# Performance work log

Hardware: AMD Instinct MI355X
Metric: run time of the kernel (lower is better)

Reference implementation:

```python
import jax, jax.numpy as jnp
from jax import lax
import numpy as np


def _conv(x, w, b, stride=1, pad=0):
    # x: NCHW, w: OIHW
    o = lax.conv_general_dilated(x, w, (stride, stride), [(pad, pad), (pad, pad)],
                                 dimension_numbers=('NCHW', 'OIHW', 'NCHW'))
    return o + b[None, :, None, None]


def _up2(x):
    return jnp.repeat(jnp.repeat(x, 2, axis=2), 2, axis=3)


def _boundary_agg(x, w, b):
    # up_to_bottom = prefix-max along H; bottom_to_up = suffix-max along H;
    # left_to_right / right_to_left (via rot90) = prefix/suffix max along W (square spatial).
    x1 = lax.cummax(x, axis=2)
    x2 = lax.cummax(x, axis=2, reverse=True)
    x3 = lax.cummax(x, axis=3)
    x4 = lax.cummax(x, axis=3, reverse=True)
    return _conv(jnp.concatenate([x, x1, x2, x3, x4], axis=1), w, b)


def _forward(C3, C4, C5,
             ba3_w, ba3_b, ba4_w, ba4_b, ba5_w, ba5_b,
             p5_1_w, p5_1_b, p5_1d_w, p5_1d_b, p5_2_w, p5_2_b,
             p4_1_w, p4_1_b, p4_1d_w, p4_1d_b, p4_2_w, p4_2_b,
             p3_1_w, p3_1_b, p3_1d_w, p3_1d_b, p3_2_w, p3_2_b,
             p6_w, p6_b, p7_w, p7_b,
             c34_w, c34_b, c45_w, c45_b, c35_w, c35_b,
             gamma3, gamma4, gamma5):
    C3_BA = _boundary_agg(C3, ba3_w, ba3_b)
    C4_BA = _boundary_agg(C4, ba4_w, ba4_b)
    C5_BA = _boundary_agg(C5, ba5_w, ba5_b)
    # top-down path
    P5 = _conv(C5, p5_1_w, p5_1_b)
    P5u1 = _up2(P5)
    P5u2 = _up2(P5u1)
    P5 = _conv(P5, p5_2_w, p5_2_b, 1, 1)
    P4 = _conv(C4, p4_1_w, p4_1_b) + P5u1
    P4u1 = _up2(P4)
    P4 = _conv(P4, p4_2_w, p4_2_b, 1, 1)
    P3 = _conv(C3, p3_1_w, p3_1_b) + P4u1 + P5u2
    P3 = _conv(P3, p3_2_w, p3_2_b, 1, 1)
    # bottom-up (dual) path on boundary-aggregated features
    P3d = _conv(C3_BA, p3_1d_w, p3_1d_b)
    P3d1 = _conv(P3d, c34_w, c34_b, 2, 1)   # 3x3 s2 p1
    P3d2 = _conv(P3d1, c35_w, c35_b, 2, 0)  # 2x2 s2 p0
    P4d = _conv(C4_BA, p4_1d_w, p4_1d_b) + P3d1
    P4d1 = _conv(P4d, c45_w, c45_b, 2, 0)   # 2x2 s2 p0
    P5d = _conv(C5_BA, p5_1d_w, p5_1d_b) + P4d1 + P3d2
    # extra levels
    P6 = _conv(C5, p6_w, p6_b, 2, 1)
    P7 = _conv(jax.nn.relu(P6), p7_w, p7_b, 2, 1)
    # gated merge
    O3 = gamma3 * P3d + (1.0 - gamma3) * P3
    O4 = gamma4 * P4d + (1.0 - gamma4) * P4
    O5 = gamma5 * P5d + (1.0 - gamma5) * P5
    return (O3, O4, O5, P6, P7)


def setup_inputs() -> dict:
    key = jax.random.key(0)
    ks = iter(jax.random.split(key, 48))
    def rnd(shape, scale):
        return jax.random.normal(next(ks), shape, dtype=jnp.float32) * scale
    B, F = 8, 256
    d = {
        'C3': rnd((B, 256, 64, 64), 1.0),
        'C4': rnd((B, 512, 32, 32), 1.0),
        'C5': rnd((B, 1024, 16, 16), 1.0),
        # Boundary_Aggregation 1x1 convs: in_channels*5 -> in_channels
        'ba3_w': rnd((256, 1280, 1, 1), 0.02), 'ba3_b': rnd((256,), 0.02),
        'ba4_w': rnd((512, 2560, 1, 1), 0.02), 'ba4_b': rnd((512,), 0.02),
        'ba5_w': rnd((1024, 5120, 1, 1), 0.01), 'ba5_b': rnd((1024,), 0.02),
        # FPN lateral / smoothing convs
        'p5_1_w': rnd((F, 1024, 1, 1), 0.02), 'p5_1_b': rnd((F,), 0.02),
        'p5_1d_w': rnd((F, 1024, 1, 1), 0.02), 'p5_1d_b': rnd((F,), 0.02),
        'p5_2_w': rnd((F, F, 3, 3), 0.02), 'p5_2_b': rnd((F,), 0.02),
        'p4_1_w': rnd((F, 512, 1, 1), 0.02), 'p4_1_b': rnd((F,), 0.02),
        'p4_1d_w': rnd((F, 512, 1, 1), 0.02), 'p4_1d_b': rnd((F,), 0.02),
        'p4_2_w': rnd((F, F, 3, 3), 0.02), 'p4_2_b': rnd((F,), 0.02),
        'p3_1_w': rnd((F, 256, 1, 1), 0.02), 'p3_1_b': rnd((F,), 0.02),
        'p3_1d_w': rnd((F, 256, 1, 1), 0.02), 'p3_1d_b': rnd((F,), 0.02),
        'p3_2_w': rnd((F, F, 3, 3), 0.02), 'p3_2_b': rnd((F,), 0.02),
        'p6_w': rnd((F, 1024, 3, 3), 0.02), 'p6_b': rnd((F,), 0.02),
        'p7_w': rnd((F, F, 3, 3), 0.02), 'p7_b': rnd((F,), 0.02),
        # downsample convs in dual path
        'c34_w': rnd((F, F, 3, 3), 0.02), 'c34_b': rnd((F,), 0.02),
        'c45_w': rnd((F, F, 2, 2), 0.02), 'c45_b': rnd((F,), 0.02),
        'c35_w': rnd((F, F, 2, 2), 0.02), 'c35_b': rnd((F,), 0.02),
        'gamma3': rnd((1,), 0.3), 'gamma4': rnd((1,), 0.3), 'gamma5': rnd((1,), 0.3),
    }
    return d


def reference(C3, C4, C5,
              ba3_w, ba3_b, ba4_w, ba4_b, ba5_w, ba5_b,
              p5_1_w, p5_1_b, p5_1d_w, p5_1d_b, p5_2_w, p5_2_b,
              p4_1_w, p4_1_b, p4_1d_w, p4_1d_b, p4_2_w, p4_2_b,
              p3_1_w, p3_1_b, p3_1d_w, p3_1d_b, p3_2_w, p3_2_b,
              p6_w, p6_b, p7_w, p7_b,
              c34_w, c34_b, c45_w, c45_b, c35_w, c35_b,
              gamma3, gamma4, gamma5):
    return _forward(C3, C4, C5,
                    ba3_w, ba3_b, ba4_w, ba4_b, ba5_w, ba5_b,
                    p5_1_w, p5_1_b, p5_1d_w, p5_1d_b, p5_2_w, p5_2_b,
                    p4_1_w, p4_1_b, p4_1d_w, p4_1d_b, p4_2_w, p4_2_b,
                    p3_1_w, p3_1_b, p3_1d_w, p3_1d_b, p3_2_w, p3_2_b,
                    p6_w, p6_b, p7_w, p7_b,
                    c34_w, c34_b, c45_w, c45_b, c35_w, c35_b,
                    gamma3, gamma4, gamma5)
```

## Files before the change

kernel.cpp:

```cpp
#include <hip/hip_runtime.h>

typedef unsigned short u16;
typedef __attribute__((ext_vector_type(8))) short s8v;
typedef __attribute__((ext_vector_type(4))) float f4v;

__device__ __forceinline__ u16 f2bf(float f) {
  unsigned int x = __float_as_uint(f);
  return (u16)((x + 0x7fffu + ((x >> 16) & 1u)) >> 16);
}
__device__ __forceinline__ float bf2f(u16 u) {
  return __uint_as_float(((unsigned int)u) << 16);
}
__device__ __forceinline__ void gload16(const void* g, void* l) {
  __builtin_amdgcn_global_load_lds(
      (const __attribute__((address_space(1))) void*)g,
      (__attribute__((address_space(3))) void*)l, 16, 0, 0);
}

struct Epi {
  const float* bias;
  const u16* r1; int r1Hp, r1pad, r1sh;
  const u16* r2; int r2Hp, r2pad, r2sh;
  const float* gamma; const u16* other; int oHp, opad, gmode;
  u16* outB; int oBHp, oBpad, oBrelu;
  float* outF;
};

__device__ __forceinline__ size_t nhwc_idx(int b, int h, int w, int Hp, int pad, int Cc, int m) {
  return (((size_t)(b * Hp + h + pad)) * Hp + (w + pad)) * Cc + m;
}

__device__ __forceinline__ void epi_apply_store(float v, int m, int b, int oh, int ow,
                                                int p, int M, int l2ohow, float g, const Epi& ep) {
  if (ep.bias) v += ep.bias[m];
  if (ep.r1) v += bf2f(ep.r1[nhwc_idx(b, oh >> ep.r1sh, ow >> ep.r1sh, ep.r1Hp, ep.r1pad, 256, m)]);
  if (ep.r2) v += bf2f(ep.r2[nhwc_idx(b, oh >> ep.r2sh, ow >> ep.r2sh, ep.r2Hp, ep.r2pad, 256, m)]);
  if (ep.gmode) {
    float o = bf2f(ep.other[nhwc_idx(b, oh, ow, ep.oHp, ep.opad, 256, m)]);
    v = (ep.gmode == 1) ? (g * o + (1.f - g) * v) : (g * v + (1.f - g) * o);
  }
  if (ep.outF) ep.outF[(((size_t)(b * M + m)) << l2ohow) + p] = v;
  if (ep.outB) {
    float w = ep.oBrelu ? fmaxf(v, 0.f) : v;
    ep.outB[nhwc_idx(b, oh, ow, ep.oBHp, ep.oBpad, M, m)] = f2bf(w);
  }
}

__device__ __forceinline__ void epi4(f4v a, int mbase, int b, int oh, int ow,
                                     int p, int M, int l2ohow, float g, const Epi& ep) {
  float v[4];
#pragma unroll
  for (int r = 0; r < 4; ++r) v[r] = a[r];
  if (ep.bias) {
    const float* bp = &ep.bias[mbase];
#pragma unroll
    for (int r = 0; r < 4; ++r) v[r] += bp[r];
  }
  if (ep.r1) {
    const u16* rp = &ep.r1[nhwc_idx(b, oh >> ep.r1sh, ow >> ep.r1sh, ep.r1Hp, ep.r1pad, 256, mbase)];
#pragma unroll
    for (int r = 0; r < 4; ++r) v[r] += bf2f(rp[r]);
  }
  if (ep.r2) {
    const u16* rp = &ep.r2[nhwc_idx(b, oh >> ep.r2sh, ow >> ep.r2sh, ep.r2Hp, ep.r2pad, 256, mbase)];
#pragma unroll
    for (int r = 0; r < 4; ++r) v[r] += bf2f(rp[r]);
  }
  if (ep.gmode) {
    const u16* op = &ep.other[nhwc_idx(b, oh, ow, ep.oHp, ep.opad, 256, mbase)];
#pragma unroll
    for (int r = 0; r < 4; ++r) {
      float o = bf2f(op[r]);
      v[r] = (ep.gmode == 1) ? (g * o + (1.f - g) * v[r]) : (g * v[r] + (1.f - g) * o);
    }
  }
  if (ep.outF) {
    float* fp = &ep.outF[(((size_t)(b * M + mbase)) << l2ohow) + p];
#pragma unroll
    for (int r = 0; r < 4; ++r) fp[(size_t)r << l2ohow] = v[r];
  }
  if (ep.outB) {
    u16* obp = &ep.outB[nhwc_idx(b, oh, ow, ep.oBHp, ep.oBpad, M, mbase)];
    ushort4 pk;
    if (ep.oBrelu) { pk.x = f2bf(fmaxf(v[0], 0.f)); pk.y = f2bf(fmaxf(v[1], 0.f));
                     pk.z = f2bf(fmaxf(v[2], 0.f)); pk.w = f2bf(fmaxf(v[3], 0.f)); }
    else { pk.x = f2bf(v[0]); pk.y = f2bf(v[1]); pk.z = f2bf(v[2]); pk.w = f2bf(v[3]); }
    *(ushort4*)obp = pk;
  }
}

struct WSeg { const float* src; u16* dst; int K, l2Cin, mode, ktiles, blk0; };
struct WTab { WSeg s[17]; };

__global__ __launch_bounds__(256) void k_cvt_w(WTab tab) {
  int bid = blockIdx.x;
  int si = 0;
#pragma unroll
  for (int i = 1; i < 17; ++i) si += (bid >= tab.s[i].blk0) ? 1 : 0;
  WSeg sg = tab.s[si];
  int rel = bid - sg.blk0;
  int m = rel / sg.ktiles;
  int kt = rel - m * sg.ktiles;
  int r = kt * 256 + threadIdx.x;
  if (r >= sg.K) return;
  int Cin = 1 << sg.l2Cin;
  int q = r >> sg.l2Cin, c = r & (Cin - 1);
  int sidx;
  if (sg.mode == 1) {
    int og = (q < 4) ? (q + 1) : 0;
    sidx = m * sg.K + og * Cin + c;
  } else {
    int KHW = sg.K >> sg.l2Cin;
    sidx = (m * Cin + c) * KHW + q;
  }
  sg.dst[(size_t)m * sg.K + r] = f2bf(sg.src[sidx]);
}

__global__ __launch_bounds__(256) void k_cvt_x(const float* __restrict__ in, u16* __restrict__ out,
                                               int C, int H, int W, int Hp, int P, int tw) {
  __shared__ u16 tile[32][33];
  const int t = threadIdx.x;
  const int b = blockIdx.z, h = blockIdx.y;
  const int tc = blockIdx.x / tw, twi = blockIdx.x - tc * tw;
  const int c0 = tc * 32, w0 = twi * 32;
#pragma unroll
  for (int r = 0; r < 4; ++r) {
    int cl = (t >> 5) * 4 + r, wl = t & 31;
    if (w0 + wl < W) tile[cl][wl] = f2bf(in[(((size_t)b * C + c0 + cl) * H + h) * W + w0 + wl]);
  }
  __syncthreads();
#pragma unroll
  for (int r = 0; r < 4; ++r) {
    int wl = (t >> 5) * 4 + r, cl = t & 31;
    if (w0 + wl < W) out[(((size_t)(b * Hp + h + P)) * Hp + (w0 + wl + P)) * C + c0 + cl] = tile[cl][wl];
  }
}

template<int S, int L2S>
__global__ __launch_bounds__(256) void k_scan2(const float* __restrict__ x,
                                               u16* __restrict__ out, int l2C) {
  __shared__ u16 pl[S][S + 1], rp[S][S + 1], rs[S][S + 1];
  const int pid = blockIdx.x;
  const size_t SS = (size_t)S * S;
  const size_t GS = ((size_t)8 << l2C) * SS;
  const float* xp = x + (size_t)pid * SS;
  u16* g0 = out + (size_t)pid * SS;
  u16* g1 = g0 + GS;
  u16* g2 = g1 + GS;
  u16* g3 = g2 + GS;
  const int t = threadIdx.x;
  for (int idx = t; idx < S * S; idx += 256)
    pl[idx >> L2S][idx & (S - 1)] = f2bf(xp[idx]);
  __syncthreads();
  if (t < S) {
    float m = -INFINITY;
    for (int h = 0; h < S; ++h) { m = fmaxf(m, bf2f(pl[h][t])); g0[h * S + t] = f2bf(m); }
  } else if (t < 2 * S) {
    int c = t - S;
    float m = -INFINITY;
    for (int h = S - 1; h >= 0; --h) { m = fmaxf(m, bf2f(pl[h][c])); g1[h * S + c] = f2bf(m); }
  } else if (t < 3 * S) {
    int h = t - 2 * S;
    float m = -INFINITY;
    for (int w = 0; w < S; ++w) { m = fmaxf(m, bf2f(pl[h][w])); rp[h][w] = f2bf(m); }
  } else if (t < 4 * S) {
    int h = t - 3 * S;
    float m = -INFINITY;
    for (int w = S - 1; w >= 0; --w) { m = fmaxf(m, bf2f(pl[h][w])); rs[h][w] = f2bf(m); }
  }
  __syncthreads();
  for (int idx = t; idx < S * S; idx += 256) {
    g2[idx] = rp[idx >> L2S][idx & (S - 1)];
    g3[idx] = rs[idx >> L2S][idx & (S - 1)];
  }
}

__global__ __launch_bounds__(256) void k_tr(const u16* __restrict__ src, u16* __restrict__ dst,
                                            int C, int S, int tw) {
  __shared__ u16 tile[32][33];
  const int t = threadIdx.x;
  const int z = blockIdx.z, h = blockIdx.y;
  const int tc = blockIdx.x / tw, twi = blockIdx.x - tc * tw;
  const int c0 = tc * 32, w0 = twi * 32;
  const size_t SS = (size_t)S * S;
  const u16* sp = src + (size_t)z * C * SS;
  u16* dp = dst + (size_t)z * SS * C;
#pragma unroll
  for (int r = 0; r < 4; ++r) {
    int cl = (t >> 5) * 4 + r, wl = t & 31;
    if (w0 + wl < S) tile[cl][wl] = sp[(size_t)(c0 + cl) * SS + h * S + w0 + wl];
  }
  __syncthreads();
#pragma unroll
  for (int r = 0; r < 4; ++r) {
    int wl = (t >> 5) * 4 + r, cl = t & 31;
    if (w0 + wl < S) dp[((size_t)(h * S + w0 + wl)) * C + c0 + cl] = tile[cl][wl];
  }
}

template<int QDIV, int KW, int STR, bool FUSE>
__global__ __launch_bounds__(256)
void k_gemm(const u16* __restrict__ X, const u16* __restrict__ X2,
            const u16* __restrict__ Wt,
            float* __restrict__ part, int C, int l2C, int Hp, int ipad,
            int l2ohow, int l2ow, int K, int Ksp, int M, int N, Epi ep) {
  __shared__ u16 Al[4096];
  __shared__ u16 Bl[8192];
  const int tid = threadIdx.x, lane = tid & 63, wid = tid >> 6;

  int ntile, mtile;
  {
    const int NT = gridDim.x, MT = gridDim.y;
    int nm = blockIdx.x + NT * blockIdx.y;
    if ((NT & 7) == 0) {
      int low = nm & 7, r = nm >> 3;
      mtile = r % MT;
      ntile = ((r / MT) << 3) + low;
    } else { ntile = blockIdx.x; mtile = blockIdx.y; }
  }
  const int n0 = ntile * 128, m0 = mtile * 64;
  const int kb = blockIdx.z * Ksp;
  const int mw = (wid >> 1) * 32, nw = (wid & 1) * 64;

  const int srow = lane >> 2;
  const int schunk = (lane & 3) ^ ((srow >> 1) & 3);

  const u16* pa0 = Wt + (size_t)(m0 + wid * 16 + srow) * K + kb + schunk * 8;

  const u16* pb0 = nullptr; const u16* pb1 = nullptr;
  int rowB[2], ohsB[2], owsB[2];
  int q = 0, cnt = 0, khs = 0, kws = 0;
#pragma unroll
  for (int j = 0; j < 2; ++j) {
    int n = n0 + wid * 32 + j * 16 + srow;
    int b = n >> l2ohow, p = n & ((1 << l2ohow) - 1);
    int oh = p >> l2ow, ow = p & ((1 << l2ow) - 1);
    if (QDIV == 1) {
      const u16* gg = X + ((size_t)(b * Hp + oh + ipad) * Hp + (ow + ipad)) * C + kb + schunk * 8;
      if (j == 0) pb0 = gg; else pb1 = gg;
    } else if (QDIV == 5) {
      rowB[j] = n;
    } else {
      rowB[j] = b * Hp; ohsB[j] = oh * STR + ipad; owsB[j] = ow * STR + ipad;
    }
  }
  if (QDIV == 5) {
    q = kb >> l2C;
    int c0 = kb & (C - 1);
    cnt = (C - c0) >> 5;
    const u16* base = (q < 4) ? (X + (((size_t)q << Hp) << l2C)) : X2;
    pb0 = base + (((size_t)rowB[0]) << l2C) + c0 + schunk * 8;
    pb1 = base + (((size_t)rowB[1]) << l2C) + c0 + schunk * 8;
  } else if (QDIV != 1) {
    q = kb >> l2C;
    int c0 = kb & (C - 1);
    cnt = (C - c0) >> 5;
    if (QDIV == 4) { khs = q >> 1; kws = q & 1; } else { khs = q / 3; kws = q - khs * 3; }
    pb0 = X + ((size_t)(rowB[0] + ohsB[0] + khs) * Hp + (owsB[0] + kws)) * C + c0 + schunk * 8;
    pb1 = X + ((size_t)(rowB[1] + ohsB[1] + khs) * Hp + (owsB[1] + kws)) * C + c0 + schunk * 8;
  }

  f4v acc[2][4];
#pragma unroll
  for (int i = 0; i < 2; ++i)
#pragma unroll
    for (int j = 0; j < 4; ++j) acc[i][j] = (f4v){0.f, 0.f, 0.f, 0.f};

  const int fr = lane & 15, kc = lane >> 4;
  const int fxor = (kc ^ ((fr >> 1) & 3)) * 8;

  auto advB = [&]() {
    if (QDIV == 1) { pb0 += 32; pb1 += 32; }
    else if (--cnt == 0) {
      ++q; cnt = C >> 5;
      if (QDIV == 5) {
        const u16* base = (q < 4) ? (X + (((size_t)q << Hp) << l2C)) : X2;
        pb0 = base + (((size_t)rowB[0]) << l2C) + schunk * 8;
        pb1 = base + (((size_t)rowB[1]) << l2C) + schunk * 8;
      } else {
        if (++kws == KW) { kws = 0; ++khs; }
        pb0 = X + ((size_t)(rowB[0] + ohsB[0] + khs) * Hp + (owsB[0] + kws)) * C + schunk * 8;
        pb1 = X + ((size_t)(rowB[1] + ohsB[1] + khs) * Hp + (owsB[1] + kws)) * C + schunk * 8;
      }
    } else { pb0 += 32; pb1 += 32; }
  };
  auto stage = [&](int buf) {
    u16* la = Al + buf * 2048 + wid * 512;
    u16* lb = Bl + buf * 4096 + wid * 1024;
    gload16(pa0, la);
    gload16(pb0, lb); gload16(pb1, lb + 512);
    pa0 += 32;
    advB();
  };

  const int nt = Ksp >> 5;
  stage(0);
  for (int t = 0; t < nt; ++t) {
    const int cur = t & 1;
    if (t + 1 < nt) {
      stage(cur ^ 1);
      asm volatile("s_waitcnt vmcnt(3)" ::: "memory");
    } else {
      asm volatile("s_waitcnt vmcnt(0)" ::: "memory");
    }
    __builtin_amdgcn_s_barrier();
    asm volatile("" ::: "memory");
    const u16* ca = Al + cur * 2048;
    const u16* cb = Bl + cur * 4096;
    s8v a[2], bv[4];
#pragma unroll
    for (int mf = 0; mf < 2; ++mf) a[mf] = *(const s8v*)&ca[(mw + mf * 16 + fr) * 32 + fxor];
#pragma unroll
    for (int nf = 0; nf < 4; ++nf) bv[nf] = *(const s8v*)&cb[(nw + nf * 16 + fr) * 32 + fxor];
#pragma unroll
    for (int mf = 0; mf < 2; ++mf)
#pragma unroll
      for (int nf = 0; nf < 4; ++nf)
        acc[mf][nf] = __builtin_amdgcn_mfma_f32_16x16x32_bf16(a[mf], bv[nf], acc[mf][nf], 0, 0, 0);
    __builtin_amdgcn_s_barrier();
    asm volatile("" ::: "memory");
  }

  const int r4 = kc * 4;
  if (FUSE) {
    float g = ep.gmode ? *ep.gamma : 0.f;
#pragma unroll
    for (int nf = 0; nf < 4; ++nf) {
      int n = n0 + nw + nf * 16 + fr;
      int b = n >> l2ohow, p = n & ((1 << l2ohow) - 1);
      int oh = p >> l2ow, ow = p & ((1 << l2ow) - 1);
#pragma unroll
      for (int mf = 0; mf < 2; ++mf)
        epi4(acc[mf][nf], m0 + mw + mf * 16 + r4, b, oh, ow, p, M, l2ohow, g, ep);
    }
  } else {
#pragma unroll
    for (int mf = 0; mf < 2; ++mf)
#pragma unroll
      for (int r = 0; r < 4; ++r) {
        int m = m0 + mw + mf * 16 + r4 + r;
        float* pr = part + ((size_t)blockIdx.z * M + m) * N + n0 + nw + fr;
#pragma unroll
        for (int nf = 0; nf < 4; ++nf) pr[nf * 16] = acc[mf][nf][r];
      }
  }
}

__global__ __launch_bounds__(256) void k_red(const float* __restrict__ part, int z, int M,
                                             int l2N, int l2ohow, int l2ow, Epi ep) {
  size_t MN = ((size_t)M) << l2N;
  int N = 1 << l2N;
  float g = ep.gmode ? *ep.gamma : 0.f;
  for (size_t e = (size_t)blockIdx.x * 256 + threadIdx.x; e < MN; e += (size_t)gridDim.x * 256) {
    float v = 0.f;
    for (int s = 0; s < z; ++s) v += part[(size_t)s * MN + e];
    int m = (int)(e >> l2N), n = (int)(e & (N - 1));
    int b = n >> l2ohow, p = n & ((1 << l2ohow) - 1);
    int oh = p >> l2ow, ow = p & ((1 << l2ow) - 1);
    epi_apply_store(v, m, b, oh, ow, p, M, l2ohow, g, ep);
  }
}

static const size_t WR_BA3 = 0, WR_BA4 = 327680, WR_BA5 = 1638400,
  WR_P51 = 6881280, WR_P51D = 7143424, WR_P52 = 7405568, WR_P41 = 7995392,
  WR_P41D = 8126464, WR_P42 = 8257536, WR_P31 = 8847360, WR_P31D = 8912896,
  WR_P32 = 8978432, WR_P6 = 9568256, WR_P7 = 11927552, WR_C34 = 12517376,
  WR_C45 = 13107200, WR_C35 = 13369344;
static const size_t O_C3N = 13631488, O_C4N = 22020096, O_C5N = 26214400,
  O_C3BA = 28311552, O_C4BA = 36700160, O_C5BA = 40894464,
  O_CAT = 42991616, O_SCR = 76546048;
static const size_t O_P3D = O_CAT, O_P3PRE = O_CAT + 8921088,
  O_P4PRE = O_CAT + 17842176, O_P3D1 = O_CAT + 20209664,
  O_P4D = O_CAT + 22306816, O_P4D1 = O_CAT + 24403968,
  O_P3D2 = O_CAT + 24928256, O_P5PRE = O_CAT + 25452544,
  O_P5S = O_CAT + 26116096, O_P6R = O_CAT + 26640384, O_C5P = O_CAT + 26845184;

extern "C" void kernel_launch(void* const* d_in, const int* in_sizes, int n_in,
                              void* d_out, int out_size, void* d_ws, size_t ws_size,
                              hipStream_t stream) {
  (void)in_sizes; (void)n_in; (void)out_size; (void)ws_size;
  const float* C3 = (const float*)d_in[0];
  const float* C4 = (const float*)d_in[1];
  const float* C5 = (const float*)d_in[2];
  const float* ba3_w = (const float*)d_in[3];  const float* ba3_b = (const float*)d_in[4];
  const float* ba4_w = (const float*)d_in[5];  const float* ba4_b = (const float*)d_in[6];
  const float* ba5_w = (const float*)d_in[7];  const float* ba5_b = (const float*)d_in[8];
  const float* p5_1_w = (const float*)d_in[9];  const float* p5_1_b = (const float*)d_in[10];
  const float* p5_1d_w = (const float*)d_in[11]; const float* p5_1d_b = (const float*)d_in[12];
  const float* p5_2_w = (const float*)d_in[13]; const float* p5_2_b = (const float*)d_in[14];
  const float* p4_1_w = (const float*)d_in[15]; const float* p4_1_b = (const float*)d_in[16];
  const float* p4_1d_w = (const float*)d_in[17]; const float* p4_1d_b = (const float*)d_in[18];
  const float* p4_2_w = (const float*)d_in[19]; const float* p4_2_b = (const float*)d_in[20];
  const float* p3_1_w = (const float*)d_in[21]; const float* p3_1_b = (const float*)d_in[22];
  const float* p3_1d_w = (const float*)d_in[23]; const float* p3_1d_b = (const float*)d_in[24];
  const float* p3_2_w = (const float*)d_in[25]; const float* p3_2_b = (const float*)d_in[26];
  const float* p6_w = (const float*)d_in[27]; const float* p6_b = (const float*)d_in[28];
  const float* p7_w = (const float*)d_in[29]; const float* p7_b = (const float*)d_in[30];
  const float* c34_w = (const float*)d_in[31]; const float* c34_b = (const float*)d_in[32];
  const float* c45_w = (const float*)d_in[33]; const float* c45_b = (const float*)d_in[34];
  const float* c35_w = (const float*)d_in[35]; const float* c35_b = (const float*)d_in[36];
  const float* g3 = (const float*)d_in[37];
  const float* g4 = (const float*)d_in[38];
  const float* g5 = (const float*)d_in[39];

  float* out = (float*)d_out;
  float* O3 = out;
  float* O4 = out + 8388608;
  float* O5 = out + 10485760;
  float* P6o = out + 11010048;
  float* P7o = out + 11141120;

  u16* wsu = (u16*)d_ws;
  u16* c3n = wsu + O_C3N;  u16* c4n = wsu + O_C4N;  u16* c5n = wsu + O_C5N;
  u16* c3ba = wsu + O_C3BA; u16* c4ba = wsu + O_C4BA; u16* c5ba = wsu + O_C5BA;
  u16* catb = wsu + O_CAT;
  u16* scr = wsu + O_SCR;
  u16* p3d = wsu + O_P3D;  u16* p3d1 = wsu + O_P3D1; u16* p3d2 = wsu + O_P3D2;
  u16* p4d = wsu + O_P4D;  u16* p4d1 = wsu + O_P4D1;
  u16* p5pre = wsu + O_P5PRE; u16* p5s = wsu + O_P5S; u16* p4pre = wsu + O_P4PRE;
  u16* p3pre = wsu + O_P3PRE; u16* p6r = wsu + O_P6R; u16* c5p = wsu + O_C5P;
  float* part = (float*)scr;
  float* partba = (float*)scr;

  const Epi enone = {nullptr, nullptr,0,0,0, nullptr,0,0,0, nullptr,nullptr,0,0,0, nullptr,0,0,0, nullptr};

  WTab tab;
  int ti = 0, blk = 0;
  auto add = [&](const float* s, size_t off, int M, int K, int l2Cin, int mode) {
    int kt = (K + 255) / 256;
    tab.s[ti].src = s; tab.s[ti].dst = wsu + off; tab.s[ti].K = K;
    tab.s[ti].l2Cin = l2Cin; tab.s[ti].mode = mode;
    tab.s[ti].ktiles = kt; tab.s[ti].blk0 = blk;
    blk += M * kt; ++ti;
  };
  add(ba3_w, WR_BA3, 256, 1280, 8, 1);
  add(ba4_w, WR_BA4, 512, 2560, 9, 1);
  add(ba5_w, WR_BA5, 1024, 5120, 10, 1);
  add(p5_1_w, WR_P51, 256, 1024, 10, 0);
  add(p5_1d_w, WR_P51D, 256, 1024, 10, 0);
  add(p5_2_w, WR_P52, 256, 2304, 8, 0);
  add(p4_1_w, WR_P41, 256, 512, 9, 0);
  add(p4_1d_w, WR_P41D, 256, 512, 9, 0);
  add(p4_2_w, WR_P42, 256, 2304, 8, 0);
  add(p3_1_w, WR_P31, 256, 256, 8, 0);
  add(p3_1d_w, WR_P31D, 256, 256, 8, 0);
  add(p3_2_w, WR_P32, 256, 2304, 8, 0);
  add(p6_w, WR_P6, 256, 9216, 10, 0);
  add(p7_w, WR_P7, 256, 2304, 8, 0);
  add(c34_w, WR_C34, 256, 2304, 8, 0);
  add(c45_w, WR_C45, 256, 1024, 8, 0);
  add(c35_w, WR_C35, 256, 1024, 8, 0);
  k_cvt_w<<<blk, 256, 0, stream>>>(tab);

  k_cvt_x<<<dim3(16,64,8), 256, 0, stream>>>(C3, c3n, 256, 64, 64, 64, 0, 2);
  k_cvt_x<<<dim3(16,32,8), 256, 0, stream>>>(C4, c4n, 512, 32, 32, 32, 0, 1);
  k_cvt_x<<<dim3(32,16,8), 256, 0, stream>>>(C5, c5n, 1024, 16, 16, 16, 0, 1);

  k_scan2<64, 6><<<2048, 256, 0, stream>>>(C3, scr, 8);
  k_tr<<<dim3(16,64,32), 256, 0, stream>>>(scr, catb, 256, 64, 2);
  {
    Epi ep = {ba3_b, nullptr,0,0,0, nullptr,0,0,0, nullptr,nullptr,0,0,0, c3ba,64,0,0, nullptr};
    k_gemm<5,1,1,true><<<dim3(256,4,1), 256, 0, stream>>>(
        catb, c3n, wsu + WR_BA3, nullptr, 256, 8, 15, 0, 12, 6, 1280, 1280, 256, 32768, ep);
  }
  k_scan2<32, 5><<<4096, 256, 0, stream>>>(C4, scr, 9);
  k_tr<<<dim3(16,32,32), 256, 0, stream>>>(scr, catb, 512, 32, 1);
  k_gemm<5,1,1,false><<<dim3(64,8,2), 256, 0, stream>>>(
      catb, c4n, wsu + WR_BA4, partba, 512, 9, 13, 0, 10, 5, 2560, 1280, 512, 8192, enone);
  {
    Epi ep = {ba4_b, nullptr,0,0,0, nullptr,0,0,0, nullptr,nullptr,0,0,0, c4ba,32,0,0, nullptr};
    k_red<<<2048, 256, 0, stream>>>(partba, 2, 512, 13, 10, 5, ep);
  }
  k_scan2<16, 4><<<8192, 256, 0, stream>>>(C5, scr, 10);
  k_tr<<<dim3(32,16,32), 256, 0, stream>>>(scr, catb, 1024, 16, 1);
  k_gemm<5,1,1,false><<<dim3(16,16,4), 256, 0, stream>>>(
      catb, c5n, wsu + WR_BA5, partba, 1024, 10, 11, 0, 8, 4, 5120, 1280, 1024, 2048, enone);
  {
    Epi ep = {ba5_b, nullptr,0,0,0, nullptr,0,0,0, nullptr,nullptr,0,0,0, c5ba,16,0,0, nullptr};
    k_red<<<2048, 256, 0, stream>>>(partba, 4, 1024, 11, 8, 4, ep);
  }

  hipMemsetAsync(p3d, 0, (size_t)8921088 * 2, stream);
  hipMemsetAsync(p3pre, 0, (size_t)8921088 * 2, stream);
  hipMemsetAsync(p4pre, 0, (size_t)2367488 * 2, stream);
  hipMemsetAsync(p5pre, 0, (size_t)663552 * 2, stream);
  hipMemsetAsync(p6r, 0, (size_t)204800 * 2, stream);
  hipMemsetAsync(c5p, 0, (size_t)2654208 * 2, stream);
  k_cvt_x<<<dim3(32,16,8), 256, 0, stream>>>(C5, c5p, 1024, 16, 16, 18, 1, 1);

  {
    Epi ep = {p3_1d_b, nullptr,0,0,0, nullptr,0,0,0, nullptr,nullptr,0,0,0, p3d,66,1,0, nullptr};
    k_gemm<1,1,1,true><<<dim3(256,4,1), 256, 0, stream>>>(
        c3ba, nullptr, wsu + WR_P31D, nullptr, 256, 0, 64, 0, 12, 6, 256, 256, 256, 32768, ep);
  }
  k_gemm<9,3,2,false><<<dim3(64,4,4), 256, 0, stream>>>(
      p3d, nullptr, wsu + WR_C34, part, 256, 8, 66, 0, 10, 5, 2304, 576, 256, 8192, enone);
  {
    Epi ep = {c34_b, nullptr,0,0,0, nullptr,0,0,0, nullptr,nullptr,0,0,0, p3d1,32,0,0, nullptr};
    k_red<<<2048, 256, 0, stream>>>(part, 4, 256, 13, 10, 5, ep);
  }
  k_gemm<4,2,2,false><<<dim3(16,4,8), 256, 0, stream>>>(
      p3d1, nullptr, wsu + WR_C35, part, 256, 8, 32, 0, 8, 4, 1024, 128, 256, 2048, enone);
  {
    Epi ep = {c35_b, nullptr,0,0,0, nullptr,0,0,0, nullptr,nullptr,0,0,0, p3d2,16,0,0, nullptr};
    k_red<<<2048, 256, 0, stream>>>(part, 8, 256, 11, 8, 4, ep);
  }
  k_gemm<1,1,1,false><<<dim3(64,4,4), 256, 0, stream>>>(
      c4ba, nullptr, wsu + WR_P41D, part, 512, 0, 32, 0, 10, 5, 512, 128, 256, 8192, enone);
  {
    Epi ep = {p4_1d_b, p3d1,32,0,0, nullptr,0,0,0, nullptr,nullptr,0,0,0, p4d,32,0,0, nullptr};
    k_red<<<2048, 256, 0, stream>>>(part, 4, 256, 13, 10, 5, ep);
  }
  k_gemm<4,2,2,false><<<dim3(16,4,8), 256, 0, stream>>>(
      p4d, nullptr, wsu + WR_C45, part, 256, 8, 32, 0, 8, 4, 1024, 128, 256, 2048, enone);
  {
    Epi ep = {c45_b, nullptr,0,0,0, nullptr,0,0,0, nullptr,nullptr,0,0,0, p4d1,16,0,0, nullptr};
    k_red<<<2048, 256, 0, stream>>>(part, 8, 256, 11, 8, 4, ep);
  }

  k_gemm<1,1,1,false><<<dim3(16,4,8), 256, 0, stream>>>(
      c5n, nullptr, wsu + WR_P51, part, 1024, 0, 16, 0, 8, 4, 1024, 128, 256, 2048, enone);
  {
    Epi ep = {p5_1_b, nullptr,0,0,0, nullptr,0,0,0, nullptr,nullptr,0,0,0, p5pre,18,1,0, nullptr};
    k_red<<<2048, 256, 0, stream>>>(part, 8, 256, 11, 8, 4, ep);
  }
  k_gemm<9,3,1,false><<<dim3(16,4,8), 256, 0, stream>>>(
      p5pre, nullptr, wsu + WR_P52, part, 256, 8, 18, 0, 8, 4, 2304, 288, 256, 2048, enone);
  {
    Epi ep = {p5_2_b, nullptr,0,0,0, nullptr,0,0,0, nullptr,nullptr,0,0,0, p5s,16,0,0, nullptr};
    k_red<<<2048, 256, 0, stream>>>(part, 8, 256, 11, 8, 4, ep);
  }
  k_gemm<1,1,1,false><<<dim3(64,4,4), 256, 0, stream>>>(
      c4n, nullptr, wsu + WR_P41, part, 512, 0, 32, 0, 10, 5, 512, 128, 256, 8192, enone);
  {
    Epi ep = {p4_1_b, p5pre,18,1,1, nullptr,0,0,0, nullptr,nullptr,0,0,0, p4pre,34,1,0, nullptr};
    k_red<<<2048, 256, 0, stream>>>(part, 4, 256, 13, 10, 5, ep);
  }
  k_gemm<9,3,1,false><<<dim3(64,4,4), 256, 0, stream>>>(
      p4pre, nullptr, wsu + WR_P42, part, 256, 8, 34, 0, 10, 5, 2304, 576, 256, 8192, enone);
  {
    Epi ep = {p4_2_b, nullptr,0,0,0, nullptr,0,0,0, g4,p4d,32,0,1, nullptr,0,0,0, O4};
    k_red<<<2048, 256, 0, stream>>>(part, 4, 256, 13, 10, 5, ep);
  }
  {
    Epi ep = {p3_1_b, p4pre,34,1,1, p5pre,18,1,2, nullptr,nullptr,0,0,0, p3pre,66,1,0, nullptr};
    k_gemm<1,1,1,true><<<dim3(256,4,1), 256, 0, stream>>>(
        c3n, nullptr, wsu + WR_P31, nullptr, 256, 0, 64, 0, 12, 6, 256, 256, 256, 32768, ep);
  }
  {
    Epi ep = {p3_2_b, nullptr,0,0,0, nullptr,0,0,0, g3,p3d,66,1,1, nullptr,0,0,0, O3};
    k_gemm<9,3,1,true><<<dim3(256,4,1), 256, 0, stream>>>(
        p3pre, nullptr, wsu + WR_P32, nullptr, 256, 8, 66, 0, 12, 6, 2304, 2304, 256, 32768, ep);
  }
  k_gemm<1,1,1,false><<<dim3(16,4,8), 256, 0, stream>>>(
      c5ba, nullptr, wsu + WR_P51D, part, 1024, 0, 16, 0, 8, 4, 1024, 128, 256, 2048, enone);
  {
    Epi ep = {p5_1d_b, p4d1,16,0,0, p3d2,16,0,0, g5,p5s,16,0,2, nullptr,0,0,0, O5};
    k_red<<<2048, 256, 0, stream>>>(part, 8, 256, 11, 8, 4, ep);
  }

  k_gemm<9,3,2,false><<<dim3(4,4,32), 256, 0, stream>>>(
      c5p, nullptr, wsu + WR_P6, part, 1024, 10, 18, 0, 6, 3, 9216, 288, 256, 512, enone);
  {
    Epi ep = {p6_b, nullptr,0,0,0, nullptr,0,0,0, nullptr,nullptr,0,0,0, p6r,10,1,1, P6o};
    k_red<<<512, 256, 0, stream>>>(part, 32, 256, 9, 6, 3, ep);
  }
  k_gemm<9,3,2,false><<<dim3(1,4,8), 256, 0, stream>>>(
      p6r, nullptr, wsu + WR_P7, part, 256, 8, 10, 0, 4, 2, 2304, 288, 256, 128, enone);
  {
    Epi ep = {p7_b, nullptr,0,0,0, nullptr,0,0,0, nullptr,nullptr,0,0,0, nullptr,0,0,0, P7o};
    k_red<<<128, 256, 0, stream>>>(part, 8, 256, 7, 4, 2, ep);
  }
}
```

Measured before the change: 763.4 us.

## Load GEMM operands directly from global into registers, dropping LDS staging

Removes the shared-memory double buffer and global_load_lds staging in the implicit-GEMM conv kernel. Each wave now loads its own A and B MFMA fragments from global memory into registers, with one-step register prefetch, and drops both barriers per K-step. The cost is redundant global/L2 traffic, because waves that share the same A or B tiles each reload them, and the per-lane 16-byte loads are less coalesced.

```diff
diff --git a/kernel.cpp b/kernel.cpp
--- a/kernel.cpp
+++ b/kernel.cpp
@@ -10,11 +10,6 @@
 }
 __device__ __forceinline__ float bf2f(u16 u) {
   return __uint_as_float(((unsigned int)u) << 16);
-}
-__device__ __forceinline__ void gload16(const void* g, void* l) {
-  __builtin_amdgcn_global_load_lds(
-      (const __attribute__((address_space(1))) void*)g,
-      (__attribute__((address_space(3))) void*)l, 16, 0, 0);
 }
 
 struct Epi {
@@ -204,8 +199,6 @@
             const u16* __restrict__ Wt,
             float* __restrict__ part, int C, int l2C, int Hp, int ipad,
             int l2ohow, int l2ow, int K, int Ksp, int M, int N, Epi ep) {
-  __shared__ u16 Al[4096];
-  __shared__ u16 Bl[8192];
   const int tid = threadIdx.x, lane = tid & 63, wid = tid >> 6;
 
   int ntile, mtile;
@@ -221,27 +214,25 @@
   const int n0 = ntile * 128, m0 = mtile * 64;
   const int kb = blockIdx.z * Ksp;
   const int mw = (wid >> 1) * 32, nw = (wid & 1) * 64;
-
-  const int srow = lane >> 2;
-  const int schunk = (lane & 3) ^ ((srow >> 1) & 3);
-
-  const u16* pa0 = Wt + (size_t)(m0 + wid * 16 + srow) * K + kb + schunk * 8;
-
-  const u16* pb0 = nullptr; const u16* pb1 = nullptr;
-  int rowB[2], ohsB[2], owsB[2];
+  const int fr = lane & 15, kc = lane >> 4;
+
+  const u16* pa0 = Wt + (size_t)(m0 + mw + fr) * K + kb + kc * 8;
+  const u16* pa1 = pa0 + (size_t)16 * K;
+
+  const u16* pb[4];
+  int rowB[4], ohsB[4], owsB[4];
   int q = 0, cnt = 0, khs = 0, kws = 0;
 #pragma unroll
-  for (int j = 0; j < 2; ++j) {
-    int n = n0 + wid * 32 + j * 16 + srow;
+  for (int nf = 0; nf < 4; ++nf) {
+    int n = n0 + nw + nf * 16 + fr;
     int b = n >> l2ohow, p = n & ((1 << l2ohow) - 1);
     int oh = p >> l2ow, ow = p & ((1 << l2ow) - 1);
     if (QDIV == 1) {
-      const u16* gg = X + ((size_t)(b * Hp + oh + ipad) * Hp + (ow + ipad)) * C + kb + schunk * 8;
-      if (j == 0) pb0 = gg; else pb1 = gg;
+      pb[nf] = X + ((size_t)(b * Hp + oh + ipad) * Hp + (ow + ipad)) * C + kb + kc * 8;
     } else if (QDIV == 5) {
-      rowB[j] = n;
+      rowB[nf] = n;
     } else {
-      rowB[j] = b * Hp; ohsB[j] = oh * STR + ipad; owsB[j] = ow * STR + ipad;
+      rowB[nf] = b * Hp; ohsB[nf] = oh * STR + ipad; owsB[nf] = ow * STR + ipad;
     }
   }
   if (QDIV == 5) {
@@ -249,15 +240,17 @@
     int c0 = kb & (C - 1);
     cnt = (C - c0) >> 5;
     const u16* base = (q < 4) ? (X + (((size_t)q << Hp) << l2C)) : X2;
-    pb0 = base + (((size_t)rowB[0]) << l2C) + c0 + schunk * 8;
-    pb1 = base + (((size_t)rowB[1]) << l2C) + c0 + schunk * 8;
+#pragma unroll
+    for (int nf = 0; nf < 4; ++nf)
+      pb[nf] = base + (((size_t)rowB[nf]) << l2C) + c0 + kc * 8;
   } else if (QDIV != 1) {
     q = kb >> l2C;
     int c0 = kb & (C - 1);
     cnt = (C - c0) >> 5;
     if (QDIV == 4) { khs = q >> 1; kws = q & 1; } else { khs = q / 3; kws = q - khs * 3; }
-    pb0 = X + ((size_t)(rowB[0] + ohsB[0] + khs) * Hp + (owsB[0] + kws)) * C + c0 + schunk * 8;
-    pb1 = X + ((size_t)(rowB[1] + ohsB[1] + khs) * Hp + (owsB[1] + kws)) * C + c0 + schunk * 8;
+#pragma unroll
+    for (int nf = 0; nf < 4; ++nf)
+      pb[nf] = X + ((size_t)(rowB[nf] + ohsB[nf] + khs) * Hp + (owsB[nf] + kws)) * C + c0 + kc * 8;
   }
 
   f4v acc[2][4];
@@ -266,60 +259,59 @@
 #pragma unroll
     for (int j = 0; j < 4; ++j) acc[i][j] = (f4v){0.f, 0.f, 0.f, 0.f};
 
-  const int fr = lane & 15, kc = lane >> 4;
-  const int fxor = (kc ^ ((fr >> 1) & 3)) * 8;
-
   auto advB = [&]() {
-    if (QDIV == 1) { pb0 += 32; pb1 += 32; }
-    else if (--cnt == 0) {
+    if (QDIV == 1) {
+#pragma unroll
+      for (int nf = 0; nf < 4; ++nf) pb[nf] += 32;
+    } else if (--cnt == 0) {
       ++q; cnt = C >> 5;
       if (QDIV == 5) {
         const u16* base = (q < 4) ? (X + (((size_t)q << Hp) << l2C)) : X2;
-        pb0 = base + (((size_t)rowB[0]) << l2C) + schunk * 8;
-        pb1 = base + (((size_t)rowB[1]) << l2C) + schunk * 8;
+#pragma unroll
+        for (int nf = 0; nf < 4; ++nf)
+          pb[nf] = base + (((size_t)rowB[nf]) << l2C) + kc * 8;
       } else {
         if (++kws == KW) { kws = 0; ++khs; }
-        pb0 = X + ((size_t)(rowB[0] + ohsB[0] + khs) * Hp + (owsB[0] + kws)) * C + schunk * 8;
-        pb1 = X + ((size_t)(rowB[1] + ohsB[1] + khs) * Hp + (owsB[1] + kws)) * C + schunk * 8;
+#pragma unroll
+        for (int nf = 0; nf < 4; ++nf)
+          pb[nf] = X + ((size_t)(rowB[nf] + ohsB[nf] + khs) * Hp + (owsB[nf] + kws)) * C + kc * 8;
       }
-    } else { pb0 += 32; pb1 += 32; }
+    } else {
+#pragma unroll
+      for (int nf = 0; nf < 4; ++nf) pb[nf] += 32;
+    }
   };
-  auto stage = [&](int buf) {
-    u16* la = Al + buf * 2048 + wid * 512;
-    u16* lb = Bl + buf * 4096 + wid * 1024;
-    gload16(pa0, la);
-    gload16(pb0, lb); gload16(pb1, lb + 512);
-    pa0 += 32;
-    advB();
-  };
 
   const int nt = Ksp >> 5;
-  stage(0);
-  for (int t = 0; t < nt; ++t) {
-    const int cur = t & 1;
-    if (t + 1 < nt) {
-      stage(cur ^ 1);
-      asm volatile("s_waitcnt vmcnt(3)" ::: "memory");
-    } else {
-      asm volatile("s_waitcnt vmcnt(0)" ::: "memory");
-    }
-    __builtin_amdgcn_s_barrier();
-    asm volatile("" ::: "memory");
-    const u16* ca = Al + cur * 2048;
-    const u16* cb = Bl + cur * 4096;
-    s8v a[2], bv[4];
-#pragma unroll
-    for (int mf = 0; mf < 2; ++mf) a[mf] = *(const s8v*)&ca[(mw + mf * 16 + fr) * 32 + fxor];
-#pragma unroll
-    for (int nf = 0; nf < 4; ++nf) bv[nf] = *(const s8v*)&cb[(nw + nf * 16 + fr) * 32 + fxor];
-#pragma unroll
-    for (int mf = 0; mf < 2; ++mf)
-#pragma unroll
-      for (int nf = 0; nf < 4; ++nf)
-        acc[mf][nf] = __builtin_amdgcn_mfma_f32_16x16x32_bf16(a[mf], bv[nf], acc[mf][nf], 0, 0, 0);
-    __builtin_amdgcn_s_barrier();
-    asm volatile("" ::: "memory");
-  }
+  s8v a0, a1, b0, b1, b2, b3;
+  a0 = *(const s8v*)pa0; a1 = *(const s8v*)pa1;
+  b0 = *(const s8v*)pb[0]; b1 = *(const s8v*)pb[1];
+  b2 = *(const s8v*)pb[2]; b3 = *(const s8v*)pb[3];
+  pa0 += 32; pa1 += 32; advB();
+  for (int t = 0; t < nt - 1; ++t) {
+    s8v c0, c1, d0, d1, d2, d3;
+    c0 = *(const s8v*)pa0; c1 = *(const s8v*)pa1;
+    d0 = *(const s8v*)pb[0]; d1 = *(const s8v*)pb[1];
+    d2 = *(const s8v*)pb[2]; d3 = *(const s8v*)pb[3];
+    pa0 += 32; pa1 += 32; advB();
+    acc[0][0] = __builtin_amdgcn_mfma_f32_16x16x32_bf16(a0, b0, acc[0][0], 0, 0, 0);
+    acc[0][1] = __builtin_amdgcn_mfma_f32_16x16x32_bf16(a0, b1, acc[0][1], 0, 0, 0);
+    acc[0][2] = __builtin_amdgcn_mfma_f32_16x16x32_bf16(a0, b2, acc[0][2], 0, 0, 0);
+    acc[0][3] = __builtin_amdgcn_mfma_f32_16x16x32_bf16(a0, b3, acc[0][3], 0, 0, 0);
+    acc[1][0] = __builtin_amdgcn_mfma_f32_16x16x32_bf16(a1, b0, acc[1][0], 0, 0, 0);
+    acc[1][1] = __builtin_amdgcn_mfma_f32_16x16x32_bf16(a1, b1, acc[1][1], 0, 0, 0);
+    acc[1][2] = __builtin_amdgcn_mfma_f32_16x16x32_bf16(a1, b2, acc[1][2], 0, 0, 0);
+    acc[1][3] = __builtin_amdgcn_mfma_f32_16x16x32_bf16(a1, b3, acc[1][3], 0, 0, 0);
+    a0 = c0; a1 = c1; b0 = d0; b1 = d1; b2 = d2; b3 = d3;
+  }
+  acc[0][0] = __builtin_amdgcn_mfma_f32_16x16x32_bf16(a0, b0, acc[0][0], 0, 0, 0);
+  acc[0][1] = __builtin_amdgcn_mfma_f32_16x16x32_bf16(a0, b1, acc[0][1], 0, 0, 0);
+  acc[0][2] = __builtin_amdgcn_mfma_f32_16x16x32_bf16(a0, b2, acc[0][2], 0, 0, 0);
+  acc[0][3] = __builtin_amdgcn_mfma_f32_16x16x32_bf16(a0, b3, acc[0][3], 0, 0, 0);
+  acc[1][0] = __builtin_amdgcn_mfma_f32_16x16x32_bf16(a1, b0, acc[1][0], 0, 0, 0);
+  acc[1][1] = __builtin_amdgcn_mfma_f32_16x16x32_bf16(a1, b1, acc[1][1], 0, 0, 0);
+  acc[1][2] = __builtin_amdgcn_mfma_f32_16x16x32_bf16(a1, b2, acc[1][2], 0, 0, 0);
+  acc[1][3] = __builtin_amdgcn_mfma_f32_16x16x32_bf16(a1, b3, acc[1][3], 0, 0, 0);
 
   const int r4 = kc * 4;
   if (FUSE) {
```

After: 1.266 ms. 65.8% more time.
